# Optimization experiments

Hardware: AMD Instinct MI355X
Metric: run time of the kernel (lower is better)

## Reference

```python
import jax, jax.numpy as jnp
import numpy as np

N_NODES = 50000
N_EDGES = 600000
N_GRAPHS = 1000


def setup_inputs() -> dict:
    key = jax.random.key(0)
    ks = jax.random.split(key, 16)
    x = jax.random.normal(ks[0], (N_NODES, 37), dtype=jnp.float32)
    edge_index = jax.random.randint(ks[1], (2, N_EDGES), 0, N_NODES, dtype=jnp.int64)
    batch = jnp.sort(jax.random.randint(ks[2], (N_NODES,), 0, N_GRAPHS, dtype=jnp.int64))

    def lin(k, fi, fo):
        s = 1.0 / np.sqrt(fi)
        kw, kb = jax.random.split(k)
        W = jax.random.uniform(kw, (fi, fo), minval=-s, maxval=s, dtype=jnp.float32)
        b = jax.random.uniform(kb, (fo,), minval=-s, maxval=s, dtype=jnp.float32)
        return W, b

    W1, b1 = lin(ks[3], 37, 64)
    W2, b2 = lin(ks[4], 64, 128)
    W3, b3 = lin(ks[5], 128, 64)
    Wf1, bf1 = lin(ks[6], 64, 128)
    Wf2, bf2 = lin(ks[7], 128, 64)
    gamma = jnp.ones((64,), jnp.float32)
    beta = jnp.zeros((64,), jnp.float32)
    return dict(x=x, edge_index=edge_index, batch=batch,
                W1=W1, b1=b1, W2=W2, b2=b2, W3=W3, b3=b3,
                Wf1=Wf1, bf1=bf1, Wf2=Wf2, bf2=bf2, gamma=gamma, beta=beta)


def _gcn_conv(x, W, b, rows, cols, norm, n_nodes):
    # PyG GCNConv: out_i = sum_j norm_ij * (x_j W) + b, over A + I edges
    h = x @ W
    msg = h[rows] * norm[:, None]          # [E+N, F_out] gather
    out = jax.ops.segment_sum(msg, cols, num_segments=n_nodes)  # scatter-add
    return out + b


def reference(x, edge_index, batch,
              W1, b1, W2, b2, W3, b3,
              Wf1, bf1, Wf2, bf2, gamma, beta):
    n = x.shape[0]
    loop = jnp.arange(n, dtype=edge_index.dtype)
    rows = jnp.concatenate([edge_index[0], loop])  # source nodes (+ self loops)
    cols = jnp.concatenate([edge_index[1], loop])  # target nodes
    deg = jax.ops.segment_sum(jnp.ones_like(cols, dtype=x.dtype), cols, num_segments=n)
    dinv = jnp.where(deg > 0, jax.lax.rsqrt(jnp.maximum(deg, 1e-12)), 0.0)
    norm = dinv[rows] * dinv[cols]

    h = jax.nn.relu(_gcn_conv(x, W1, b1, rows, cols, norm, n))
    h = jax.nn.relu(_gcn_conv(h, W2, b2, rows, cols, norm, n))
    h = jax.nn.relu(_gcn_conv(h, W3, b3, rows, cols, norm, n))

    # global mean pool per graph
    sums = jax.ops.segment_sum(h, batch, num_segments=N_GRAPHS)
    cnts = jax.ops.segment_sum(jnp.ones((n,), h.dtype), batch, num_segments=N_GRAPHS)
    g = sums / jnp.maximum(cnts, 1.0)[:, None]

    g = jax.nn.relu(g @ Wf1 + bf1)
    g = jax.nn.relu(g @ Wf2 + bf2)

    mu = jnp.mean(g, axis=-1, keepdims=True)
    var = jnp.mean(jnp.square(g - mu), axis=-1, keepdims=True)
    return (g - mu) * jax.lax.rsqrt(var + 1e-5) * gamma + beta
```

## Files before the change

kernel.cpp:

```cpp
#include <hip/hip_runtime.h>
#include <hip/hip_bf16.h>


#define WAVE 64


__global__ void hist_kernel(const int* __restrict__ cols, int* __restrict__ counts, int E,
                            const int* __restrict__ batch, int* __restrict__ gcnt, int n) {
    int idx = blockIdx.x * 256 + threadIdx.x;
    if (idx < E) {
        atomicAdd(&counts[cols[idx]], 1);
    } else {
        int i = idx - E;
        if (i < n) atomicAdd(&gcnt[batch[i]], 1);
    }
}


__global__ void scan1_kernel(const int* __restrict__ counts, int* __restrict__ offs,
                             int* __restrict__ bsum, int n) {
    __shared__ int tmp[1024];
    int i = blockIdx.x * 1024 + threadIdx.x;
    int v = (i < n) ? counts[i] : 0;
    tmp[threadIdx.x] = v;
    __syncthreads();
    for (int o = 1; o < 1024; o <<= 1) {
        int x = (threadIdx.x >= o) ? tmp[threadIdx.x - o] : 0;
        __syncthreads();
        tmp[threadIdx.x] += x;
        __syncthreads();
    }
    if (i < n) offs[i] = tmp[threadIdx.x] - v;
    if (threadIdx.x == 1023) bsum[blockIdx.x] = tmp[1023];
}

__global__ void scan_meta_kernel(int* __restrict__ bsum, int nb,
                                 const int* __restrict__ gcnt, int* __restrict__ goff,
                                 int ng, int n_nodes) {
    __shared__ int ta[1024];
    __shared__ int tb[1024];
    int t = threadIdx.x;
    int va = (t < nb) ? bsum[t] : 0;
    int vb = (t < ng) ? gcnt[t] : 0;
    ta[t] = va;
    tb[t] = vb;
    __syncthreads();
    for (int o = 1; o < 1024; o <<= 1) {
        int xa = (t >= o) ? ta[t - o] : 0;
        int xb = (t >= o) ? tb[t - o] : 0;
        __syncthreads();
        ta[t] += xa;
        tb[t] += xb;
        __syncthreads();
    }
    if (t < nb) bsum[t] = ta[t] - va;
    if (t < ng) goff[t] = tb[t] - vb;
    if (t == 0) goff[ng] = n_nodes;
}

__global__ void scan3_kernel(int* __restrict__ offs, const int* __restrict__ bsum,
                             const int* __restrict__ counts, float* __restrict__ dinv,
                             int n, int E) {
    int i = blockIdx.x * 256 + threadIdx.x;
    if (i < n) {
        offs[i] += bsum[i >> 10];
        dinv[i] = rsqrtf((float)(counts[i] + 1));
    }
    if (i == 0) offs[n] = E;
}

__global__ void fill_kernel(const int* __restrict__ rows, const int* __restrict__ cols,
                            const int* __restrict__ offs, int* __restrict__ cursor,
                            const float* __restrict__ dinv,
                            int* __restrict__ esrc, float* __restrict__ enorm, int E) {
    int e = blockIdx.x * 256 + threadIdx.x;
    if (e >= E) return;
    int r = rows[e], c = cols[e];
    int pos = offs[c] + atomicAdd(&cursor[c], 1);
    esrc[pos]  = r;
    enorm[pos] = dinv[r] * dinv[c];
}


template <int K, int F>
__global__ void mm_kernel(const float* __restrict__ X, const float* __restrict__ W,
                          float* __restrict__ out, int n) {
    constexpr int ROWS = 32;
    constexpr int CG = F / 4;
    __shared__ __align__(16) float Ws[K * F];
    __shared__ __align__(16) float xs[ROWS * K];
    int r0 = blockIdx.x * ROWS;
    for (int i = threadIdx.x; i < K * F; i += 256) Ws[i] = W[i];
    int nrow = n - r0; if (nrow > ROWS) nrow = ROWS;
    const float* Xb = X + (size_t)r0 * K;
    int tot = nrow * K;
    for (int i = threadIdx.x; i < tot; i += 256) xs[i] = Xb[i];
    __syncthreads();
    for (int idx = threadIdx.x; idx < ROWS * CG; idx += 256) {
        int r = idx / CG, cg = idx % CG;
        if (r >= nrow) break;
        float4 acc = {0.f, 0.f, 0.f, 0.f};
#pragma unroll
        for (int k = 0; k < K; ++k) {
            float xv = xs[r * K + k];
            float4 wv = *reinterpret_cast<const float4*>(&Ws[k * F + cg * 4]);
            acc.x += xv * wv.x; acc.y += xv * wv.y;
            acc.z += xv * wv.z; acc.w += xv * wv.w;
        }
        *reinterpret_cast<float4*>(&out[(size_t)(r0 + r) * F + cg * 4]) = acc;
    }
}


template <int K, int F, int BR, int KC>
__global__ __launch_bounds__(256)
void mm_tiled_kernel(const float* __restrict__ X, const float* __restrict__ W,
                     float* __restrict__ out, int n) {
    constexpr int TC = F / 4;
    constexpr int TR = 256 / TC;
    constexpr int R  = BR / TR;
    constexpr int XS = KC + 4;
    static_assert(R == 8, "tile math assumes 8 rows/thread");
    static_assert(K % KC == 0 && KC % 4 == 0, "bad K chunking");

    __shared__ __align__(16) float Ws[K * F];
    __shared__ __align__(16) float xs[BR * XS];

    const int t  = threadIdx.x;
    const int tc = t % TC;
    const int tr = t / TC;
    const int r0 = blockIdx.x * BR;

    for (int i = t * 4; i < K * F; i += 1024)
        *reinterpret_cast<float4*>(&Ws[i]) = *reinterpret_cast<const float4*>(&W[i]);

    float4 acc[R];
#pragma unroll
    for (int i = 0; i < R; ++i) acc[i] = float4{0.f, 0.f, 0.f, 0.f};

    for (int kc = 0; kc < K; kc += KC) {
        __syncthreads();
        constexpr int VPR = KC / 4;
        for (int idx = t; idx < BR * VPR; idx += 256) {
            int row = idx / VPR, col = idx % VPR;
            int gr = r0 + row; if (gr >= n) gr = n - 1;
            *reinterpret_cast<float4*>(&xs[row * XS + col * 4]) =
                *reinterpret_cast<const float4*>(&X[(size_t)gr * K + kc + col * 4]);
        }
        __syncthreads();

#pragma unroll 2
        for (int kk = 0; kk < KC; kk += 4) {
            float4 xv[R];
#pragma unroll
            for (int i = 0; i < R; ++i)
                xv[i] = *reinterpret_cast<const float4*>(&xs[(tr + TR * i) * XS + kk]);
            float4 wv[4];
#pragma unroll
            for (int j = 0; j < 4; ++j)
                wv[j] = *reinterpret_cast<const float4*>(&Ws[(kc + kk + j) * F + tc * 4]);
#pragma unroll
            for (int i = 0; i < R; ++i) {
                const float* xp = reinterpret_cast<const float*>(&xv[i]);
#pragma unroll
                for (int j = 0; j < 4; ++j) {
                    float s = xp[j];
                    acc[i].x += s * wv[j].x;
                    acc[i].y += s * wv[j].y;
                    acc[i].z += s * wv[j].z;
                    acc[i].w += s * wv[j].w;
                }
            }
        }
    }

#pragma unroll
    for (int i = 0; i < R; ++i) {
        int gr = r0 + tr + TR * i;
        if (gr < n)
            *reinterpret_cast<float4*>(&out[(size_t)gr * F + tc * 4]) = acc[i];
    }
}


template <int F>
__global__ void agg_kernel(const float* __restrict__ h, const int* __restrict__ offs,
                           const int* __restrict__ esrc, const float* __restrict__ enorm,
                           const float* __restrict__ dinv, const float* __restrict__ bias,
                           float* __restrict__ out, int n) {
    constexpr int J = F / WAVE;
    int wid  = threadIdx.x >> 6;
    int lane = threadIdx.x & 63;
    int node = blockIdx.x * 4 + wid;
    if (node >= n) return;
    float dv = dinv[node];
    float sn = dv * dv;
    float acc0[J], acc1[J];
#pragma unroll
    for (int j = 0; j < J; ++j) {
        acc0[j] = sn * h[(size_t)node * F + lane + 64 * j];
        acc1[j] = 0.f;
    }
    int s = offs[node], e = offs[node + 1];
    int k = s;
    for (; k + 1 < e; k += 2) {
        int   s0 = esrc[k],  s1 = esrc[k + 1];
        float w0 = enorm[k], w1 = enorm[k + 1];
#pragma unroll
        for (int j = 0; j < J; ++j) {
            acc0[j] += w0 * h[(size_t)s0 * F + lane + 64 * j];
            acc1[j] += w1 * h[(size_t)s1 * F + lane + 64 * j];
        }
    }
    if (k < e) {
        int   s0 = esrc[k];
        float w0 = enorm[k];
#pragma unroll
        for (int j = 0; j < J; ++j)
            acc0[j] += w0 * h[(size_t)s0 * F + lane + 64 * j];
    }
#pragma unroll
    for (int j = 0; j < J; ++j) {
        float v = acc0[j] + acc1[j] + bias[lane + 64 * j];
        out[(size_t)node * F + lane + 64 * j] = v > 0.f ? v : 0.f;
    }
}


__global__ void gpool_kernel(const float* __restrict__ h, const int* __restrict__ goff,
                             float* __restrict__ gmean, int ng) {
    int wid = threadIdx.x >> 6, lane = threadIdx.x & 63;
    int g = blockIdx.x * 4 + wid;
    if (g >= ng) return;
    int s = goff[g], e = goff[g + 1];
    float acc = 0.f;
    for (int i = s; i < e; ++i) acc += h[(size_t)i * 64 + lane];
    float c = (float)(e - s);
    gmean[g * 64 + lane] = acc / fmaxf(c, 1.0f);
}


__global__ void mlp_kernel(const float* __restrict__ gmean,
                           const float* __restrict__ Wf1, const float* __restrict__ bf1,
                           const float* __restrict__ Wf2, const float* __restrict__ bf2,
                           const float* __restrict__ gamma, const float* __restrict__ beta,
                           float* __restrict__ out) {
    __shared__ float gs[64];
    __shared__ float ts[128];
    int g = blockIdx.x, t = threadIdx.x;
    if (t < 64) gs[t] = gmean[g * 64 + t];
    __syncthreads();
    float acc = bf1[t];
    for (int k = 0; k < 64; ++k) acc += gs[k] * Wf1[k * 128 + t];
    ts[t] = fmaxf(acc, 0.f);
    __syncthreads();
    if (t < 64) {
        float acc2 = bf2[t];
        for (int k = 0; k < 128; ++k) acc2 += ts[k] * Wf2[k * 64 + t];
        float u = fmaxf(acc2, 0.f);
        float mu = u;
        for (int o = 1; o < 64; o <<= 1) mu += __shfl_xor(mu, o);
        mu *= (1.0f / 64.0f);
        float d = u - mu;
        float var = d * d;
        for (int o = 1; o < 64; o <<= 1) var += __shfl_xor(var, o);
        var *= (1.0f / 64.0f);
        out[g * 64 + t] = d * rsqrtf(var + 1e-5f) * gamma[t] + beta[t];
    }
}


extern "C" void kernel_launch(void* const* d_in, const int* in_sizes, int n_in,
                              void* d_out, int out_size, void* d_ws, size_t ws_size,
                              hipStream_t stream) {
    const float* x     = (const float*)d_in[0];
    const int*   eidx  = (const int*)d_in[1];
    const int*   batch = (const int*)d_in[2];
    const float* W1 = (const float*)d_in[3];  const float* b1 = (const float*)d_in[4];
    const float* W2 = (const float*)d_in[5];  const float* b2 = (const float*)d_in[6];
    const float* W3 = (const float*)d_in[7];  const float* b3 = (const float*)d_in[8];
    const float* Wf1 = (const float*)d_in[9];  const float* bf1 = (const float*)d_in[10];
    const float* Wf2 = (const float*)d_in[11]; const float* bf2 = (const float*)d_in[12];
    const float* gamma = (const float*)d_in[13]; const float* beta = (const float*)d_in[14];
    float* out = (float*)d_out;

    const int n  = in_sizes[2];
    const int E  = in_sizes[1] / 2;
    const int ng = out_size / 64;
    const int NB = (n + 1023) / 1024;

    const int* rows = eidx;
    const int* cols = eidx + E;

    size_t off = 0;
    auto carve = [&](size_t bytes) {
        void* p = (char*)d_ws + off;
        off += (bytes + 511) & ~(size_t)511;
        return p;
    };
    int*   counts = (int*)  carve((size_t)n * 4);
    int*   cursor = (int*)  carve((size_t)n * 4);
    int*   gcnt   = (int*)  carve((size_t)(ng + 1) * 4);
    size_t zbytes = off;
    int*   offs   = (int*)  carve((size_t)(n + 1) * 4);
    int*   bsum   = (int*)  carve((size_t)(NB + 1) * 4);
    float* dinv   = (float*)carve((size_t)n * 4);
    int*   esrc   = (int*)  carve((size_t)E * 4);
    float* enorm  = (float*)carve((size_t)E * 4);
    float* bufA   = (float*)carve((size_t)n * 128 * 4);
    float* bufB   = (float*)carve((size_t)n * 128 * 4);
    int*   goff   = (int*)  carve((size_t)(ng + 1) * 4);
    float* gmean  = (float*)carve((size_t)ng * 64 * 4);
    (void)ws_size;

    hipMemsetAsync(d_ws, 0, zbytes, stream);

    int gH = (E + n + 255) / 256;
    hist_kernel<<<gH, 256, 0, stream>>>(cols, counts, E, batch, gcnt, n);
    scan1_kernel<<<NB, 1024, 0, stream>>>(counts, offs, bsum, n);
    scan_meta_kernel<<<1, 1024, 0, stream>>>(bsum, NB, gcnt, goff, ng, n);
    scan3_kernel<<<(n + 255) / 256, 256, 0, stream>>>(offs, bsum, counts, dinv, n, E);
    fill_kernel<<<(E + 255) / 256, 256, 0, stream>>>(rows, cols, offs, cursor, dinv,
                                                     esrc, enorm, E);

    int gagg = (n + 3) / 4;
    mm_kernel<37, 64><<<(n + 31) / 32, 256, 0, stream>>>(x, W1, bufA, n);
    agg_kernel<64><<<gagg, 256, 0, stream>>>(bufA, offs, esrc, enorm, dinv, b1, bufB, n);
    mm_tiled_kernel<64, 128, 64, 64><<<(n + 63) / 64, 256, 0, stream>>>(bufB, W2, bufA, n);
    agg_kernel<128><<<gagg, 256, 0, stream>>>(bufA, offs, esrc, enorm, dinv, b2, bufB, n);
    mm_tiled_kernel<128, 64, 128, 64><<<(n + 127) / 128, 256, 0, stream>>>(bufB, W3, bufA, n);
    agg_kernel<64><<<gagg, 256, 0, stream>>>(bufA, offs, esrc, enorm, dinv, b3, bufB, n);

    gpool_kernel<<<(ng + 3) / 4, 256, 0, stream>>>(bufB, goff, gmean, ng);
    mlp_kernel<<<ng, 128, 0, stream>>>(gmean, Wf1, bf1, Wf2, bf2, gamma, beta, out);
}
```

Measured before the change: 382.5 us.

## Reorder GCN aggregate/matmul and fold symmetric norm into per-node scaling

Applies the symmetric normalization as per-node dinv scaling before and after aggregation, so the per-edge enorm array and its loads go away. Layer 1 now aggregates the 37-wide input before the matmul. Layers 2 and 3 chain their matmuls so only 64-wide features are gathered, never 128-wide; bias, ReLU and dinv scaling are fused into the matmul epilogues. Pooling and the MLP become a single kernel, and the aggregation loop unrolls by four neighbours. The risk is the extra scale kernel and a non-power-of-two 37-wide gather with clamped lanes.

```diff
diff --git a/kernel.cpp b/kernel.cpp
--- a/kernel.cpp
+++ b/kernel.cpp
@@ -5,8 +5,9 @@
 #define WAVE 64
 
 
-__global__ void hist_kernel(const int* __restrict__ cols, int* __restrict__ counts, int E,
-                            const int* __restrict__ batch, int* __restrict__ gcnt, int n) {
+__global__ __launch_bounds__(256)
+void hist_kernel(const int* __restrict__ cols, int* __restrict__ counts, int E,
+                 const int* __restrict__ batch, int* __restrict__ gcnt, int n) {
     int idx = blockIdx.x * 256 + threadIdx.x;
     if (idx < E) {
         atomicAdd(&counts[cols[idx]], 1);
@@ -17,8 +18,9 @@
 }
 
 
-__global__ void scan1_kernel(const int* __restrict__ counts, int* __restrict__ offs,
-                             int* __restrict__ bsum, int n) {
+__global__ __launch_bounds__(1024)
+void scan1_kernel(const int* __restrict__ counts, int* __restrict__ offs,
+                  int* __restrict__ bsum, int n) {
     __shared__ int tmp[1024];
     int i = blockIdx.x * 1024 + threadIdx.x;
     int v = (i < n) ? counts[i] : 0;
@@ -34,9 +36,10 @@
     if (threadIdx.x == 1023) bsum[blockIdx.x] = tmp[1023];
 }
 
-__global__ void scan_meta_kernel(int* __restrict__ bsum, int nb,
-                                 const int* __restrict__ gcnt, int* __restrict__ goff,
-                                 int ng, int n_nodes) {
+__global__ __launch_bounds__(1024)
+void scan_meta_kernel(int* __restrict__ bsum, int nb,
+                      const int* __restrict__ gcnt, int* __restrict__ goff,
+                      int ng, int n_nodes) {
     __shared__ int ta[1024];
     __shared__ int tb[1024];
     int t = threadIdx.x;
@@ -58,9 +61,10 @@
     if (t == 0) goff[ng] = n_nodes;
 }
 
-__global__ void scan3_kernel(int* __restrict__ offs, const int* __restrict__ bsum,
-                             const int* __restrict__ counts, float* __restrict__ dinv,
-                             int n, int E) {
+__global__ __launch_bounds__(256)
+void scan3_kernel(int* __restrict__ offs, const int* __restrict__ bsum,
+                  const int* __restrict__ counts, float* __restrict__ dinv,
+                  int n, int E) {
     int i = blockIdx.x * 256 + threadIdx.x;
     if (i < n) {
         offs[i] += bsum[i >> 10];
@@ -69,22 +73,85 @@
     if (i == 0) offs[n] = E;
 }
 
-__global__ void fill_kernel(const int* __restrict__ rows, const int* __restrict__ cols,
-                            const int* __restrict__ offs, int* __restrict__ cursor,
-                            const float* __restrict__ dinv,
-                            int* __restrict__ esrc, float* __restrict__ enorm, int E) {
+__global__ __launch_bounds__(256)
+void fill_kernel(const int* __restrict__ rows, const int* __restrict__ cols,
+                 const int* __restrict__ offs, int* __restrict__ cursor,
+                 int* __restrict__ esrc, int E) {
     int e = blockIdx.x * 256 + threadIdx.x;
     if (e >= E) return;
     int r = rows[e], c = cols[e];
     int pos = offs[c] + atomicAdd(&cursor[c], 1);
-    esrc[pos]  = r;
-    enorm[pos] = dinv[r] * dinv[c];
+    esrc[pos] = r;
+}
+
+
+template <int F>
+__global__ __launch_bounds__(256)
+void scale_kernel(const float* __restrict__ x, const float* __restrict__ dinv,
+                  float* __restrict__ g0, int total) {
+    int i = blockIdx.x * 256 + threadIdx.x;
+    if (i < total) g0[i] = x[i] * dinv[i / F];
+}
+
+
+template <int F>
+__global__ __launch_bounds__(256)
+void agg_kernel(const float* __restrict__ g, const int* __restrict__ offs,
+                const int* __restrict__ esrc, const float* __restrict__ dinv,
+                const float* __restrict__ bias, int do_relu,
+                float* __restrict__ out, int n) {
+    constexpr int J = (F + 63) / 64;
+    int wid  = threadIdx.x >> 6;
+    int lane = threadIdx.x & 63;
+    int node = blockIdx.x * 4 + wid;
+    if (node >= n) return;
+    float acc0[J], acc1[J], acc2[J], acc3[J];
+#pragma unroll
+    for (int j = 0; j < J; ++j) {
+        int c = lane + 64 * j; if (F % 64 && c >= F) c = F - 1;
+        acc0[j] = g[(size_t)node * F + c];
+        acc1[j] = 0.f; acc2[j] = 0.f; acc3[j] = 0.f;
+    }
+    int s = offs[node], e = offs[node + 1];
+    int k = s;
+    for (; k + 3 < e; k += 4) {
+        int s0 = esrc[k], s1 = esrc[k + 1], s2 = esrc[k + 2], s3 = esrc[k + 3];
+#pragma unroll
+        for (int j = 0; j < J; ++j) {
+            int c = lane + 64 * j; if (F % 64 && c >= F) c = F - 1;
+            acc0[j] += g[(size_t)s0 * F + c];
+            acc1[j] += g[(size_t)s1 * F + c];
+            acc2[j] += g[(size_t)s2 * F + c];
+            acc3[j] += g[(size_t)s3 * F + c];
+        }
+    }
+    for (; k < e; ++k) {
+        int s0 = esrc[k];
+#pragma unroll
+        for (int j = 0; j < J; ++j) {
+            int c = lane + 64 * j; if (F % 64 && c >= F) c = F - 1;
+            acc0[j] += g[(size_t)s0 * F + c];
+        }
+    }
+    float dv = dinv[node];
+#pragma unroll
+    for (int j = 0; j < J; ++j) {
+        int c = lane + 64 * j;
+        if (F % 64 == 0 || c < F) {
+            float v = ((acc0[j] + acc1[j]) + (acc2[j] + acc3[j])) * dv;
+            if (bias)    v += bias[c];
+            if (do_relu) v = fmaxf(v, 0.f);
+            out[(size_t)node * F + c] = v;
+        }
+    }
 }
 
 
 template <int K, int F>
-__global__ void mm_kernel(const float* __restrict__ X, const float* __restrict__ W,
-                          float* __restrict__ out, int n) {
+__global__ __launch_bounds__(256)
+void mm_kernel(const float* __restrict__ X, const float* __restrict__ W,
+               const float* __restrict__ bias, const float* __restrict__ dscale,
+               int do_relu, float* __restrict__ out, int n) {
     constexpr int ROWS = 32;
     constexpr int CG = F / 4;
     __shared__ __align__(16) float Ws[K * F];
@@ -107,6 +174,18 @@
             acc.x += xv * wv.x; acc.y += xv * wv.y;
             acc.z += xv * wv.z; acc.w += xv * wv.w;
         }
+        if (bias) {
+            const float4 bv = *reinterpret_cast<const float4*>(&bias[cg * 4]);
+            acc.x += bv.x; acc.y += bv.y; acc.z += bv.z; acc.w += bv.w;
+        }
+        if (do_relu) {
+            acc.x = fmaxf(acc.x, 0.f); acc.y = fmaxf(acc.y, 0.f);
+            acc.z = fmaxf(acc.z, 0.f); acc.w = fmaxf(acc.w, 0.f);
+        }
+        if (dscale) {
+            float dv = dscale[r0 + r];
+            acc.x *= dv; acc.y *= dv; acc.z *= dv; acc.w *= dv;
+        }
         *reinterpret_cast<float4*>(&out[(size_t)(r0 + r) * F + cg * 4]) = acc;
     }
 }
@@ -115,7 +194,8 @@
 template <int K, int F, int BR, int KC>
 __global__ __launch_bounds__(256)
 void mm_tiled_kernel(const float* __restrict__ X, const float* __restrict__ W,
-                     float* __restrict__ out, int n) {
+                     const float* __restrict__ bias, const float* __restrict__ dscale,
+                     int do_relu, float* __restrict__ out, int n) {
     constexpr int TC = F / 4;
     constexpr int TR = 256 / TC;
     constexpr int R  = BR / TR;
@@ -174,90 +254,57 @@
         }
     }
 
+    float4 bv = {0.f, 0.f, 0.f, 0.f};
+    if (bias) bv = *reinterpret_cast<const float4*>(&bias[tc * 4]);
 #pragma unroll
     for (int i = 0; i < R; ++i) {
         int gr = r0 + tr + TR * i;
-        if (gr < n)
-            *reinterpret_cast<float4*>(&out[(size_t)gr * F + tc * 4]) = acc[i];
-    }
-}
-
-
-template <int F>
-__global__ void agg_kernel(const float* __restrict__ h, const int* __restrict__ offs,
-                           const int* __restrict__ esrc, const float* __restrict__ enorm,
-                           const float* __restrict__ dinv, const float* __restrict__ bias,
-                           float* __restrict__ out, int n) {
-    constexpr int J = F / WAVE;
-    int wid  = threadIdx.x >> 6;
-    int lane = threadIdx.x & 63;
-    int node = blockIdx.x * 4 + wid;
-    if (node >= n) return;
-    float dv = dinv[node];
-    float sn = dv * dv;
-    float acc0[J], acc1[J];
-#pragma unroll
-    for (int j = 0; j < J; ++j) {
-        acc0[j] = sn * h[(size_t)node * F + lane + 64 * j];
-        acc1[j] = 0.f;
-    }
-    int s = offs[node], e = offs[node + 1];
-    int k = s;
-    for (; k + 1 < e; k += 2) {
-        int   s0 = esrc[k],  s1 = esrc[k + 1];
-        float w0 = enorm[k], w1 = enorm[k + 1];
-#pragma unroll
-        for (int j = 0; j < J; ++j) {
-            acc0[j] += w0 * h[(size_t)s0 * F + lane + 64 * j];
-            acc1[j] += w1 * h[(size_t)s1 * F + lane + 64 * j];
-        }
-    }
-    if (k < e) {
-        int   s0 = esrc[k];
-        float w0 = enorm[k];
-#pragma unroll
-        for (int j = 0; j < J; ++j)
-            acc0[j] += w0 * h[(size_t)s0 * F + lane + 64 * j];
-    }
-#pragma unroll
-    for (int j = 0; j < J; ++j) {
-        float v = acc0[j] + acc1[j] + bias[lane + 64 * j];
-        out[(size_t)node * F + lane + 64 * j] = v > 0.f ? v : 0.f;
-    }
-}
-
-
-__global__ void gpool_kernel(const float* __restrict__ h, const int* __restrict__ goff,
-                             float* __restrict__ gmean, int ng) {
-    int wid = threadIdx.x >> 6, lane = threadIdx.x & 63;
-    int g = blockIdx.x * 4 + wid;
-    if (g >= ng) return;
-    int s = goff[g], e = goff[g + 1];
-    float acc = 0.f;
-    for (int i = s; i < e; ++i) acc += h[(size_t)i * 64 + lane];
-    float c = (float)(e - s);
-    gmean[g * 64 + lane] = acc / fmaxf(c, 1.0f);
-}
-
-
-__global__ void mlp_kernel(const float* __restrict__ gmean,
-                           const float* __restrict__ Wf1, const float* __restrict__ bf1,
-                           const float* __restrict__ Wf2, const float* __restrict__ bf2,
-                           const float* __restrict__ gamma, const float* __restrict__ beta,
-                           float* __restrict__ out) {
+        if (gr < n) {
+            float4 v = acc[i];
+            if (bias) { v.x += bv.x; v.y += bv.y; v.z += bv.z; v.w += bv.w; }
+            if (do_relu) {
+                v.x = fmaxf(v.x, 0.f); v.y = fmaxf(v.y, 0.f);
+                v.z = fmaxf(v.z, 0.f); v.w = fmaxf(v.w, 0.f);
+            }
+            if (dscale) {
+                float dv = dscale[gr];
+                v.x *= dv; v.y *= dv; v.z *= dv; v.w *= dv;
+            }
+            *reinterpret_cast<float4*>(&out[(size_t)gr * F + tc * 4]) = v;
+        }
+    }
+}
+
+
+__global__ __launch_bounds__(128)
+void poolmlp_kernel(const float* __restrict__ h, const int* __restrict__ goff,
+                    const float* __restrict__ Wf1, const float* __restrict__ bf1,
+                    const float* __restrict__ Wf2, const float* __restrict__ bf2,
+                    const float* __restrict__ gamma, const float* __restrict__ beta,
+                    float* __restrict__ out) {
+    __shared__ float red[128];
     __shared__ float gs[64];
     __shared__ float ts[128];
     int g = blockIdx.x, t = threadIdx.x;
-    if (t < 64) gs[t] = gmean[g * 64 + t];
-    __syncthreads();
-    float acc = bf1[t];
-    for (int k = 0; k < 64; ++k) acc += gs[k] * Wf1[k * 128 + t];
-    ts[t] = fmaxf(acc, 0.f);
+    int f = t & 63, half = t >> 6;
+    int s = goff[g], e = goff[g + 1];
+    float acc = 0.f;
+    for (int i = s + half; i < e; i += 2) acc += h[(size_t)i * 64 + f];
+    red[t] = acc;
     __syncthreads();
     if (t < 64) {
-        float acc2 = bf2[t];
-        for (int k = 0; k < 128; ++k) acc2 += ts[k] * Wf2[k * 64 + t];
-        float u = fmaxf(acc2, 0.f);
+        float c = (float)(e - s);
+        gs[t] = (red[t] + red[t + 64]) / fmaxf(c, 1.0f);
+    }
+    __syncthreads();
+    float a1 = bf1[t];
+    for (int k = 0; k < 64; ++k) a1 += gs[k] * Wf1[k * 128 + t];
+    ts[t] = fmaxf(a1, 0.f);
+    __syncthreads();
+    if (t < 64) {
+        float a2 = bf2[t];
+        for (int k = 0; k < 128; ++k) a2 += ts[k] * Wf2[k * 64 + t];
+        float u = fmaxf(a2, 0.f);
         float mu = u;
         for (int o = 1; o < 64; o <<= 1) mu += __shfl_xor(mu, o);
         mu *= (1.0f / 64.0f);
@@ -306,11 +353,9 @@
     int*   bsum   = (int*)  carve((size_t)(NB + 1) * 4);
     float* dinv   = (float*)carve((size_t)n * 4);
     int*   esrc   = (int*)  carve((size_t)E * 4);
-    float* enorm  = (float*)carve((size_t)E * 4);
+    int*   goff   = (int*)  carve((size_t)(ng + 1) * 4);
     float* bufA   = (float*)carve((size_t)n * 128 * 4);
-    float* bufB   = (float*)carve((size_t)n * 128 * 4);
-    int*   goff   = (int*)  carve((size_t)(ng + 1) * 4);
-    float* gmean  = (float*)carve((size_t)ng * 64 * 4);
+    float* bufB   = (float*)carve((size_t)n * 64 * 4);
     (void)ws_size;
 
     hipMemsetAsync(d_ws, 0, zbytes, stream);
@@ -320,17 +365,18 @@
     scan1_kernel<<<NB, 1024, 0, stream>>>(counts, offs, bsum, n);
     scan_meta_kernel<<<1, 1024, 0, stream>>>(bsum, NB, gcnt, goff, ng, n);
     scan3_kernel<<<(n + 255) / 256, 256, 0, stream>>>(offs, bsum, counts, dinv, n, E);
-    fill_kernel<<<(E + 255) / 256, 256, 0, stream>>>(rows, cols, offs, cursor, dinv,
-                                                     esrc, enorm, E);
+    scale_kernel<37><<<(n * 37 + 255) / 256, 256, 0, stream>>>(x, dinv, bufA, n * 37);
+    fill_kernel<<<(E + 255) / 256, 256, 0, stream>>>(rows, cols, offs, cursor, esrc, E);
 
     int gagg = (n + 3) / 4;
-    mm_kernel<37, 64><<<(n + 31) / 32, 256, 0, stream>>>(x, W1, bufA, n);
-    agg_kernel<64><<<gagg, 256, 0, stream>>>(bufA, offs, esrc, enorm, dinv, b1, bufB, n);
-    mm_tiled_kernel<64, 128, 64, 64><<<(n + 63) / 64, 256, 0, stream>>>(bufB, W2, bufA, n);
-    agg_kernel<128><<<gagg, 256, 0, stream>>>(bufA, offs, esrc, enorm, dinv, b2, bufB, n);
-    mm_tiled_kernel<128, 64, 128, 64><<<(n + 127) / 128, 256, 0, stream>>>(bufB, W3, bufA, n);
-    agg_kernel<64><<<gagg, 256, 0, stream>>>(bufA, offs, esrc, enorm, dinv, b3, bufB, n);
-
-    gpool_kernel<<<(ng + 3) / 4, 256, 0, stream>>>(bufB, goff, gmean, ng);
-    mlp_kernel<<<ng, 128, 0, stream>>>(gmean, Wf1, bf1, Wf2, bf2, gamma, beta, out);
-}
+    agg_kernel<37><<<gagg, 256, 0, stream>>>(bufA, offs, esrc, dinv, nullptr, 0, bufB, n);
+    mm_kernel<37, 64><<<(n + 31) / 32, 256, 0, stream>>>(bufB, W1, b1, dinv, 1, bufA, n);
+    agg_kernel<64><<<gagg, 256, 0, stream>>>(bufA, offs, esrc, dinv, nullptr, 0, bufB, n);
+    mm_tiled_kernel<64, 128, 64, 64><<<(n + 63) / 64, 256, 0, stream>>>(
+        bufB, W2, b2, nullptr, 1, bufA, n);
+    mm_tiled_kernel<128, 64, 128, 64><<<(n + 127) / 128, 256, 0, stream>>>(
+        bufA, W3, nullptr, dinv, 0, bufB, n);
+    agg_kernel<64><<<gagg, 256, 0, stream>>>(bufB, offs, esrc, dinv, b3, 1, bufA, n);
+
+    poolmlp_kernel<<<ng, 128, 0, stream>>>(bufA, goff, Wf1, bf1, Wf2, bf2, gamma, beta, out);
+}
```

Result: faster. 343.0 us (-10.3%).
